# Kernel tuning notes

Hardware: AMD Instinct MI355X
Metric: run time of the kernel (lower is better)

## Reference

```python
import jax, jax.numpy as jnp
import numpy as np

# Grid derived from defaults: pc_range=(0,-40,-3,70.4,40,1), voxel=(0.2,0.2,4)
GX, GY = 352, 400          # round((70.4-0)/0.2), round((40-(-40))/0.2)
B, P = 4, 65536            # samples, points per sample
NSEG = B * GX * GY + 1     # dense pillar-id space + 1 sentinel for masked points
OUT_CH = 64
BN_EPS = 1e-3


def setup_inputs() -> dict:
    key = jax.random.key(0)
    k1, k2, k3 = jax.random.split(key, 3)
    xyz_min = jnp.array([0.0, -40.0, -3.0], jnp.float32)
    xyz_max = jnp.array([70.4, 40.0, 1.0], jnp.float32)
    xyz = jax.random.uniform(k1, (B, P, 3), jnp.float32, minval=xyz_min, maxval=xyz_max)
    rest = jax.random.normal(k2, (B, P, 4), jnp.float32)  # rcs, v_r, v_r_comp, time
    points = jnp.concatenate([xyz, rest], axis=-1)        # [B, P, 7]
    W = jax.random.normal(k3, (OUT_CH, 13), jnp.float32) * (1.0 / np.sqrt(13.0))
    gamma = jnp.ones((OUT_CH,), jnp.float32)
    beta = jnp.zeros((OUT_CH,), jnp.float32)
    return {"points": points, "W": W, "gamma": gamma, "beta": beta}


def reference(points, W, gamma, beta):
    Bn, Pn, _ = points.shape
    pts = points.reshape(Bn * Pn, 7)                      # [N, 7] (= torch points[:, 1:])
    dtype = pts.dtype
    voxel = jnp.array([0.2, 0.2, 4.0], dtype)
    pc_min = jnp.array([0.0, -40.0, -3.0], dtype)
    batch_idx = jnp.repeat(jnp.arange(Bn, dtype=jnp.int32), Pn)

    coords_f = (pts[:, :3] - pc_min) / voxel              # float voxel coords
    mask = ((coords_f[:, 0] >= 0) & (coords_f[:, 0] < GX)
            & (coords_f[:, 1] >= 0) & (coords_f[:, 1] < GY))
    coords = coords_f.astype(jnp.int32)                   # [N, 3] (cx, cy, cz)
    sentinel = Bn * GX * GY                               # trash segment for masked points
    lin = jnp.where(mask,
                    batch_idx * (GX * GY) + coords[:, 0] * GY + coords[:, 1],
                    sentinel)
    # torch.unique(..., return_inverse=True, dim=0) on (batch, cx, cy) rows ==
    # unique of the bijective linear id (same sorted order).
    unq, unq_inv = jnp.unique(lin, return_inverse=True, size=NSEG, fill_value=sentinel)

    cnt = jax.ops.segment_sum(jnp.ones((lin.shape[0], 1), dtype), unq_inv, num_segments=NSEG)
    mean_xyz = jax.ops.segment_sum(pts[:, :3], unq_inv, num_segments=NSEG) / jnp.maximum(cnt, 1.0)
    f_cluster = pts[:, :3] - mean_xyz[unq_inv]
    f_center = pts[:, :3] - (coords.astype(dtype) * voxel + voxel * 0.5 + pc_min)
    feats = jnp.concatenate([pts, f_cluster, f_center], axis=-1)   # [N, 13]

    # PFN layer (last_layer=True): Linear -> BN1d (training stats) -> ReLU
    x = feats @ W.T                                       # [N, 64]
    mu = x.mean(axis=0)
    var = x.var(axis=0)                                   # biased, as BN training
    x = jax.nn.relu((x - mu) * jax.lax.rsqrt(var + BN_EPS) * gamma + beta)

    fmax = jax.ops.segment_max(x, unq_inv, num_segments=NSEG)     # scatter_max
    x_max = fmax[unq_inv]                                 # gather back (PFN output)
    feat_max = jax.ops.segment_max(x_max, unq_inv, num_segments=NSEG)

    valid = (unq < sentinel)[:, None]                     # real pillars only
    feat_max = jnp.where(valid, feat_max, 0.0)            # padded/empty -> 0

    b = unq // (GX * GY)
    rem = unq % (GX * GY)
    cx = rem // GY
    cy = rem % GY
    coords_out = jnp.stack([b, cy, cx], axis=1).astype(jnp.int32)  # (batch, y, x)
    grid_size = jnp.array([GY, GX], jnp.int32)
    return feat_max, coords_out, grid_size
```

## Files before the change

### kernel.cpp

```cpp
#include <hip/hip_runtime.h>
#include <stdint.h>
#include <utility>

#define NPTS   262144
#define GXGY   140800
#define GYv    400
#define NSEG   563201
#define SENT   563200
#define NB_SCAN 275
#define PIL_BLOCKS 2048
#define MOM_BLOCKS 512

constexpr size_t alignup(size_t x) { return (x + 255) & ~(size_t)255; }
constexpr size_t O_CNT  = 0;
constexpr size_t O_SUMS = alignup(O_CNT + (size_t)NSEG * 4);
constexpr size_t O_MOM  = alignup(O_SUMS + (size_t)NSEG * 12);
constexpr size_t ZERO_BYTES = alignup(O_MOM + 104 * 4);
constexpr size_t O_PPTR = ZERO_BYTES;
constexpr size_t O_LINA = alignup(O_PPTR + (size_t)NSEG * 4);
constexpr size_t O_ROWI = alignup(O_LINA + (size_t)NPTS * 4);
constexpr size_t O_FEAT = alignup(O_ROWI + (size_t)NPTS * 16);
constexpr size_t O_BSO  = alignup(O_FEAT + (size_t)NPTS * 64);
constexpr size_t O_BSC  = alignup(O_BSO + NB_SCAN * 4);
constexpr size_t O_KP   = alignup(O_BSC + NB_SCAN * 4);
constexpr size_t O_WF   = alignup(O_KP + 256);
constexpr size_t O_SH   = alignup(O_WF + 832 * 4);

__device__ __forceinline__ int point_lin(float x, float y, int b, bool& mask) {
  float cxf = x / 0.2f;
  float cyf = (y + 40.0f) / 0.2f;
  int cx = (int)cxf, cy = (int)cyf;
  mask = (cxf >= 0.0f) && (cxf < 352.0f) && (cyf >= 0.0f) && (cyf < 400.0f);
  return mask ? (b * GXGY + cx * GYv + cy) : SENT;
}

__global__ __launch_bounds__(256) void k_count(const float* __restrict__ pts,
                                               unsigned int* __restrict__ cnt,
                                               float* __restrict__ sums,
                                               unsigned int* __restrict__ lina) {
  int i = blockIdx.x * 256 + threadIdx.x;
  if (i >= NPTS) return;
  const float* p = pts + (size_t)i * 7;
  float x = p[0], y = p[1], z = p[2];
  bool m;
  int lin = point_lin(x, y, i >> 16, m);
  lina[i] = (unsigned)lin;
  atomicAdd(&cnt[lin], 1u);
  atomicAdd(&sums[lin * 3 + 0], x);
  atomicAdd(&sums[lin * 3 + 1], y);
  atomicAdd(&sums[lin * 3 + 2], z);
}

__global__ __launch_bounds__(256) void k_scan1(const unsigned int* __restrict__ cnt,
                                               unsigned int* __restrict__ bso,
                                               unsigned int* __restrict__ bsc) {
  int t = threadIdx.x;
  int base = blockIdx.x * 2048 + t * 8;
  const uint4* c4 = (const uint4*)(cnt + base);
  uint4 a = c4[0], b = c4[1];
  unsigned so = (a.x > 0) + (a.y > 0) + (a.z > 0) + (a.w > 0) +
                (b.x > 0) + (b.y > 0) + (b.z > 0) + (b.w > 0);
  unsigned sc = a.x + a.y + a.z + a.w + b.x + b.y + b.z + b.w;
  for (int m = 1; m < 64; m <<= 1) { so += __shfl_xor(so, m); sc += __shfl_xor(sc, m); }
  __shared__ unsigned wo[4], wc[4];
  if ((t & 63) == 0) { wo[t >> 6] = so; wc[t >> 6] = sc; }
  __syncthreads();
  if (t == 0) {
    bso[blockIdx.x] = wo[0] + wo[1] + wo[2] + wo[3];
    bsc[blockIdx.x] = wc[0] + wc[1] + wc[2] + wc[3];
  }
}

__global__ __launch_bounds__(256) void k_scan3(const unsigned int* __restrict__ cnt,
                                               const unsigned int* __restrict__ bso,
                                               const unsigned int* __restrict__ bsc,
                                               uint4* __restrict__ rowinfo,
                                               unsigned int* __restrict__ pptr,
                                               unsigned int* __restrict__ kp) {
  int t = threadIdx.x;
  unsigned vo_m = 0, vc_m = 0, vo_a = 0;
  for (int e = t; e < NB_SCAN; e += 256) {
    unsigned o = bso[e], c = bsc[e];
    vo_a += o;
    if (e < (int)blockIdx.x) { vo_m += o; vc_m += c; }
  }
  for (int m = 1; m < 64; m <<= 1) {
    vo_m += __shfl_xor(vo_m, m);
    vc_m += __shfl_xor(vc_m, m);
    vo_a += __shfl_xor(vo_a, m);
  }
  __shared__ unsigned s0[4], s1[4], s2[4];
  int wv = t >> 6;
  if ((t & 63) == 0) { s0[wv] = vo_m; s1[wv] = vc_m; s2[wv] = vo_a; }
  __syncthreads();
  unsigned boo = s0[0] + s0[1] + s0[2] + s0[3];
  unsigned boc = s1[0] + s1[1] + s1[2] + s1[3];
  unsigned tot = s2[0] + s2[1] + s2[2] + s2[3];
  if (blockIdx.x == 0 && t == 0) *kp = tot;

  int base = blockIdx.x * 2048 + t * 8;
  const uint4* q = (const uint4*)(cnt + base);
  uint4 a = q[0], b = q[1];
  unsigned c[8] = {a.x, a.y, a.z, a.w, b.x, b.y, b.z, b.w};
  unsigned po[8], pc[8];
  unsigned so = 0, sc = 0;
#pragma unroll
  for (int k = 0; k < 8; k++) {
    po[k] = so; pc[k] = sc;
    so += (c[k] > 0); sc += c[k];
  }
  __shared__ unsigned sdo[256], sdc[256];
  __syncthreads();
  sdo[t] = so; sdc[t] = sc;
  __syncthreads();
  for (int off = 1; off < 256; off <<= 1) {
    unsigned ao = (t >= off) ? sdo[t - off] : 0u;
    unsigned ac = (t >= off) ? sdc[t - off] : 0u;
    __syncthreads();
    sdo[t] += ao; sdc[t] += ac;
    __syncthreads();
  }
  unsigned eo = sdo[t] - so + boo;
  unsigned ec = sdc[t] - sc + boc;
#pragma unroll
  for (int k = 0; k < 8; k++) {
    if (c[k] > 0) {
      unsigned r = eo + po[k];
      unsigned start = ec + pc[k];
      rowinfo[r] = make_uint4((unsigned)(base + k), start, c[k], 0u);
      pptr[base + k] = start;
    }
  }
}

__global__ __launch_bounds__(256) void k_sortfeat(const float* __restrict__ pts,
                                                  const unsigned int* __restrict__ lina,
                                                  const unsigned int* __restrict__ cnt,
                                                  const float* __restrict__ sums,
                                                  unsigned int* __restrict__ pptr,
                                                  float* __restrict__ feat) {
  int i = blockIdx.x * 256 + threadIdx.x;
  if (i >= NPTS) return;
  unsigned lin = lina[i];
  if (lin == SENT) return;
  const float* p = pts + (size_t)i * 7;
  float x = p[0], y = p[1], z = p[2];
  unsigned pos = atomicAdd(&pptr[lin], 1u);
  float cm = fmaxf((float)cnt[lin], 1.0f);
  float m0 = sums[lin * 3 + 0] / cm;
  float m1 = sums[lin * 3 + 1] / cm;
  float m2 = sums[lin * 3 + 2] / cm;
  int cx = (int)(x / 0.2f);
  int cy = (int)((y + 40.0f) / 0.2f);
  int cz = (int)((z + 3.0f) / 4.0f);
  float4 A = make_float4(x, y, z, p[3]);
  float4 B = make_float4(p[4], p[5], p[6], x - m0);
  float4 C = make_float4(y - m1, z - m2,
                         x - ((float)cx * 0.2f + 0.1f + 0.0f),
                         y - ((float)cy * 0.2f + 0.1f - 40.0f));
  float4 D = make_float4(z - ((float)cz * 4.0f + 2.0f - 3.0f), 0.f, 0.f, 0.f);
  float4* fb = (float4*)(feat + (size_t)pos * 16);
  fb[0] = A; fb[1] = B; fb[2] = C; fb[3] = D;
}

constexpr int tri_j(int t) { int j = 0; while (t >= 13 - j) { t -= 13 - j; j++; } return j; }
constexpr int tri_k(int t) { int j = 0; while (t >= 13 - j) { t -= 13 - j; j++; } return j + t; }

template<int G, size_t U>
__device__ __forceinline__ void accum_one(const float (&f)[13], float (&acc)[52]) {
  constexpr int E = G * 52 + (int)U;
  if constexpr (E < 13) {
    acc[U] += f[E];
  } else {
    constexpr int J = tri_j(E - 13);
    constexpr int K = tri_k(E - 13);
    acc[U] += f[J] * f[K];
  }
}
template<int G, size_t... Us>
__device__ __forceinline__ void accum_all(const float (&f)[13], float (&acc)[52],
                                          std::index_sequence<Us...>) {
  (accum_one<G, Us>(f, acc), ...);
}

template<int G>
__device__ __forceinline__ void moments_body(const float* __restrict__ feat,
                                             float* __restrict__ mom, int chunk) {
  float acc[52];
#pragma unroll
  for (int u = 0; u < 52; u++) acc[u] = 0.f;
#pragma unroll
  for (int r = 0; r < 4; r++) {
    int i = chunk * 1024 + r * 256 + threadIdx.x;
    const float4* fp = (const float4*)(feat + (size_t)i * 16);
    float4 A = fp[0], B = fp[1], C = fp[2], D = fp[3];
    float f[13] = {A.x, A.y, A.z, A.w, B.x, B.y, B.z, B.w, C.x, C.y, C.z, C.w, D.x};
    accum_all<G>(f, acc, std::make_index_sequence<52>{});
  }
  __shared__ float red[4][52];
  int wv = threadIdx.x >> 6, lane = threadIdx.x & 63;
#pragma unroll
  for (int u = 0; u < 52; u++) {
    float v = acc[u];
    v += __shfl_xor(v, 1);  v += __shfl_xor(v, 2);  v += __shfl_xor(v, 4);
    v += __shfl_xor(v, 8);  v += __shfl_xor(v, 16); v += __shfl_xor(v, 32);
    if (lane == 0) red[wv][u] = v;
  }
  __syncthreads();
  if (threadIdx.x < 52) {
    int u = threadIdx.x;
    atomicAdd(&mom[G * 52 + u], red[0][u] + red[1][u] + red[2][u] + red[3][u]);
  }
}

__global__ __launch_bounds__(256, 2) void k_moments(const float* __restrict__ feat,
                                                    float* __restrict__ mom) {
  int chunk = blockIdx.x >> 1;
  if ((blockIdx.x & 1) == 0) moments_body<0>(feat, mom, chunk);
  else                       moments_body<1>(feat, mom, chunk);
}

__global__ void k_bnfinal(const float* __restrict__ W,
                          const float* __restrict__ g,
                          const float* __restrict__ bta,
                          const float* __restrict__ mom,
                          float* __restrict__ wf,
                          float* __restrict__ sh) {
  int c = threadIdx.x;
  float w[13];
#pragma unroll
  for (int j = 0; j < 13; j++) w[j] = W[c * 13 + j];
  const float invN = 1.0f / (float)NPTS;
  float mu = 0.f;
#pragma unroll
  for (int j = 0; j < 13; j++) mu += w[j] * (mom[j] * invN);
  float e2 = 0.f;
  int mi = 13;
#pragma unroll
  for (int j = 0; j < 13; j++) {
#pragma unroll
    for (int k = j; k < 13; k++) {
      float coef = (j == k) ? 1.0f : 2.0f;
      e2 += coef * w[j] * w[k] * mom[mi];
      mi++;
    }
  }
  e2 *= invN;
  float var = e2 - mu * mu;
  float rsig = 1.0f / sqrtf(var + 1e-3f);
  float sc = g[c] * rsig;
#pragma unroll
  for (int j = 0; j < 13; j++) wf[c * 13 + j] = w[j] * sc;
  sh[c] = bta[c] - mu * sc;
}

__global__ __launch_bounds__(256) void k_pillar(const float* __restrict__ wf,
                                                const float* __restrict__ sh,
                                                const uint4* __restrict__ rowinfo,
                                                const unsigned int* __restrict__ kp_p,
                                                const float* __restrict__ feat,
                                                float* __restrict__ out) {
  int tid = threadIdx.x;
  int lane = tid & 15;
  int ch0 = lane * 4;
  float wr[52];
  float shv[4];
#pragma unroll
  for (int c4 = 0; c4 < 4; c4++) {
    shv[c4] = sh[ch0 + c4];
#pragma unroll
    for (int j = 0; j < 13; j++) wr[c4 * 13 + j] = wf[(ch0 + c4) * 13 + j];
  }
  unsigned kp = *kp_p;

  const int NGRP = PIL_BLOCKS * 16;
  for (int r = blockIdx.x * 16 + (tid >> 4); r < NSEG; r += NGRP) {
    float m0 = -3.4e38f, m1 = -3.4e38f, m2 = -3.4e38f, m3 = -3.4e38f;
    int b = 4, cy = 0, cx = 0;
    if ((unsigned)r < kp) {
      uint4 ri = rowinfo[r];
      unsigned id = ri.x, start = ri.y, n = ri.z;
      b = id / GXGY;
      unsigned rem = id - (unsigned)b * GXGY;
      cx = rem / GYv;
      cy = rem - cx * GYv;
      const float4* fb = (const float4*)(feat + (size_t)start * 16);
      for (unsigned p = 0; p < n; p++) {
        float4 A = fb[0], B = fb[1], C = fb[2], D = fb[3];
        fb += 4;
        float d0, d1, d2, d3;
#define DOT(dst, c4)                                                          \
        dst = shv[c4];                                                        \
        dst += wr[c4 * 13 + 0]  * A.x;  dst += wr[c4 * 13 + 1]  * A.y;        \
        dst += wr[c4 * 13 + 2]  * A.z;  dst += wr[c4 * 13 + 3]  * A.w;        \
        dst += wr[c4 * 13 + 4]  * B.x;  dst += wr[c4 * 13 + 5]  * B.y;        \
        dst += wr[c4 * 13 + 6]  * B.z;  dst += wr[c4 * 13 + 7]  * B.w;        \
        dst += wr[c4 * 13 + 8]  * C.x;  dst += wr[c4 * 13 + 9]  * C.y;        \
        dst += wr[c4 * 13 + 10] * C.z;  dst += wr[c4 * 13 + 11] * C.w;        \
        dst += wr[c4 * 13 + 12] * D.x;
        DOT(d0, 0) DOT(d1, 1) DOT(d2, 2) DOT(d3, 3)
#undef DOT
        m0 = fmaxf(m0, d0); m1 = fmaxf(m1, d1);
        m2 = fmaxf(m2, d2); m3 = fmaxf(m3, d3);
      }
    }
    float4 v = make_float4(fmaxf(m0, 0.f), fmaxf(m1, 0.f),
                           fmaxf(m2, 0.f), fmaxf(m3, 0.f));
    *(float4*)(out + (size_t)r * 64 + lane * 4) = v;
    if (lane == 0) {
      float* cc = out + (size_t)NSEG * 64 + (size_t)r * 3;
      cc[0] = (float)b;
      cc[1] = (float)cy;
      cc[2] = (float)cx;
    }
  }
  if (blockIdx.x == 0 && tid == 0) {
    float* g = out + (size_t)NSEG * 67;
    g[0] = 400.0f;
    g[1] = 352.0f;
  }
}

extern "C" void kernel_launch(void* const* d_in, const int* in_sizes, int n_in,
                              void* d_out, int out_size, void* d_ws, size_t ws_size,
                              hipStream_t stream) {
  const float* pts = (const float*)d_in[0];
  const float* W   = (const float*)d_in[1];
  const float* g   = (const float*)d_in[2];
  const float* bta = (const float*)d_in[3];
  float* out = (float*)d_out;
  char* ws = (char*)d_ws;

  unsigned int* cnt  = (unsigned int*)(ws + O_CNT);
  float*        sums = (float*)(ws + O_SUMS);
  float*        mom  = (float*)(ws + O_MOM);
  unsigned int* pptr = (unsigned int*)(ws + O_PPTR);
  unsigned int* lina = (unsigned int*)(ws + O_LINA);
  uint4*        rowi = (uint4*)(ws + O_ROWI);
  float*        feat = (float*)(ws + O_FEAT);
  unsigned int* bso  = (unsigned int*)(ws + O_BSO);
  unsigned int* bsc  = (unsigned int*)(ws + O_BSC);
  unsigned int* kp   = (unsigned int*)(ws + O_KP);
  float*        wf   = (float*)(ws + O_WF);
  float*        sh   = (float*)(ws + O_SH);
  (void)in_sizes; (void)n_in; (void)out_size; (void)ws_size;

  hipMemsetAsync(ws, 0, ZERO_BYTES, stream);

  k_count   <<<NPTS / 256, 256, 0, stream>>>(pts, cnt, sums, lina);
  k_scan1   <<<NB_SCAN, 256, 0, stream>>>(cnt, bso, bsc);
  k_scan3   <<<NB_SCAN, 256, 0, stream>>>(cnt, bso, bsc, rowi, pptr, kp);
  k_sortfeat<<<NPTS / 256, 256, 0, stream>>>(pts, lina, cnt, sums, pptr, feat);
  k_moments <<<MOM_BLOCKS, 256, 0, stream>>>(feat, mom);
  k_bnfinal <<<1, 64, 0, stream>>>(W, g, bta, mom, wf, sh);
  k_pillar  <<<PIL_BLOCKS, 256, 0, stream>>>(wf, sh, rowi, kp, feat, out);
}
```

Baseline: 286.9 us.

## Compute pillar means from sorted points and fold derived features into weights

Drops the float atomic scatter of xyz sums and the lina buffer. k_sortfeat now stores only the raw 7-channel point in a 32-byte record. Pillar means are computed per pillar inside the moments kernel, which walks sorted rows and rebuilds the 13 features on the fly. k_pillar folds the cluster and center offsets into per-pillar bias terms and combined weights, so each point needs fewer FMAs and half the feature bytes. The risk is load imbalance, because the moments kernel now iterates per pillar with a variable point count, and the float summation order changes.

```diff
diff --git a/kernel.cpp b/kernel.cpp
--- a/kernel.cpp
+++ b/kernel.cpp
@@ -9,18 +9,17 @@
 #define SENT   563200
 #define NB_SCAN 275
 #define PIL_BLOCKS 2048
-#define MOM_BLOCKS 512
+#define MOMG_BLOCKS 512
 
 constexpr size_t alignup(size_t x) { return (x + 255) & ~(size_t)255; }
 constexpr size_t O_CNT  = 0;
-constexpr size_t O_SUMS = alignup(O_CNT + (size_t)NSEG * 4);
-constexpr size_t O_MOM  = alignup(O_SUMS + (size_t)NSEG * 12);
+constexpr size_t O_MOM  = alignup(O_CNT + (size_t)NSEG * 4);
 constexpr size_t ZERO_BYTES = alignup(O_MOM + 104 * 4);
 constexpr size_t O_PPTR = ZERO_BYTES;
-constexpr size_t O_LINA = alignup(O_PPTR + (size_t)NSEG * 4);
-constexpr size_t O_ROWI = alignup(O_LINA + (size_t)NPTS * 4);
+constexpr size_t O_ROWI = alignup(O_PPTR + (size_t)NSEG * 4);
 constexpr size_t O_FEAT = alignup(O_ROWI + (size_t)NPTS * 16);
-constexpr size_t O_BSO  = alignup(O_FEAT + (size_t)NPTS * 64);
+constexpr size_t O_MEAN = alignup(O_FEAT + (size_t)NPTS * 32);
+constexpr size_t O_BSO  = alignup(O_MEAN + (size_t)NPTS * 12);
 constexpr size_t O_BSC  = alignup(O_BSO + NB_SCAN * 4);
 constexpr size_t O_KP   = alignup(O_BSC + NB_SCAN * 4);
 constexpr size_t O_WF   = alignup(O_KP + 256);
@@ -35,20 +34,14 @@
 }
 
 __global__ __launch_bounds__(256) void k_count(const float* __restrict__ pts,
-                                               unsigned int* __restrict__ cnt,
-                                               float* __restrict__ sums,
-                                               unsigned int* __restrict__ lina) {
+                                               unsigned int* __restrict__ cnt) {
   int i = blockIdx.x * 256 + threadIdx.x;
   if (i >= NPTS) return;
   const float* p = pts + (size_t)i * 7;
-  float x = p[0], y = p[1], z = p[2];
+  float x = p[0], y = p[1];
   bool m;
   int lin = point_lin(x, y, i >> 16, m);
-  lina[i] = (unsigned)lin;
   atomicAdd(&cnt[lin], 1u);
-  atomicAdd(&sums[lin * 3 + 0], x);
-  atomicAdd(&sums[lin * 3 + 1], y);
-  atomicAdd(&sums[lin * 3 + 2], z);
 }
 
 __global__ __launch_bounds__(256) void k_scan1(const unsigned int* __restrict__ cnt,
@@ -134,33 +127,19 @@
 }
 
 __global__ __launch_bounds__(256) void k_sortfeat(const float* __restrict__ pts,
-                                                  const unsigned int* __restrict__ lina,
-                                                  const unsigned int* __restrict__ cnt,
-                                                  const float* __restrict__ sums,
                                                   unsigned int* __restrict__ pptr,
                                                   float* __restrict__ feat) {
   int i = blockIdx.x * 256 + threadIdx.x;
   if (i >= NPTS) return;
-  unsigned lin = lina[i];
-  if (lin == SENT) return;
   const float* p = pts + (size_t)i * 7;
   float x = p[0], y = p[1], z = p[2];
+  bool m;
+  int lin = point_lin(x, y, i >> 16, m);
+  if (lin == SENT) return;
   unsigned pos = atomicAdd(&pptr[lin], 1u);
-  float cm = fmaxf((float)cnt[lin], 1.0f);
-  float m0 = sums[lin * 3 + 0] / cm;
-  float m1 = sums[lin * 3 + 1] / cm;
-  float m2 = sums[lin * 3 + 2] / cm;
-  int cx = (int)(x / 0.2f);
-  int cy = (int)((y + 40.0f) / 0.2f);
-  int cz = (int)((z + 3.0f) / 4.0f);
-  float4 A = make_float4(x, y, z, p[3]);
-  float4 B = make_float4(p[4], p[5], p[6], x - m0);
-  float4 C = make_float4(y - m1, z - m2,
-                         x - ((float)cx * 0.2f + 0.1f + 0.0f),
-                         y - ((float)cy * 0.2f + 0.1f - 40.0f));
-  float4 D = make_float4(z - ((float)cz * 4.0f + 2.0f - 3.0f), 0.f, 0.f, 0.f);
-  float4* fb = (float4*)(feat + (size_t)pos * 16);
-  fb[0] = A; fb[1] = B; fb[2] = C; fb[3] = D;
+  float4* fb = (float4*)(feat + (size_t)pos * 8);
+  fb[0] = make_float4(x, y, z, p[3]);
+  fb[1] = make_float4(p[4], p[5], p[6], 0.0f);
 }
 
 constexpr int tri_j(int t) { int j = 0; while (t >= 13 - j) { t -= 13 - j; j++; } return j; }
@@ -184,18 +163,41 @@
 }
 
 template<int G>
-__device__ __forceinline__ void moments_body(const float* __restrict__ feat,
-                                             float* __restrict__ mom, int chunk) {
+__device__ __forceinline__ void momrank_body(const uint4* __restrict__ rowinfo,
+                                             const float* __restrict__ feat,
+                                             float* __restrict__ meanr,
+                                             float* __restrict__ mom,
+                                             unsigned kp) {
   float acc[52];
 #pragma unroll
   for (int u = 0; u < 52; u++) acc[u] = 0.f;
-#pragma unroll
-  for (int r = 0; r < 4; r++) {
-    int i = chunk * 1024 + r * 256 + threadIdx.x;
-    const float4* fp = (const float4*)(feat + (size_t)i * 16);
-    float4 A = fp[0], B = fp[1], C = fp[2], D = fp[3];
-    float f[13] = {A.x, A.y, A.z, A.w, B.x, B.y, B.z, B.w, C.x, C.y, C.z, C.w, D.x};
-    accum_all<G>(f, acc, std::make_index_sequence<52>{});
+  const unsigned stride = MOMG_BLOCKS * 256;
+  for (unsigned r = (blockIdx.x >> 1) * 256 + threadIdx.x; r < kp; r += stride) {
+    uint4 ri = rowinfo[r];
+    unsigned start = ri.y, n = ri.z;
+    const float4* fp = (const float4*)(feat + (size_t)start * 8);
+    float sx = 0.f, sy = 0.f, sz = 0.f;
+    for (unsigned p = 0; p < n; p++) { float4 A = fp[2 * p]; sx += A.x; sy += A.y; sz += A.z; }
+    float inv = 1.0f / fmaxf((float)n, 1.0f);
+    float mx = sx * inv, my = sy * inv, mz = sz * inv;
+    if (G == 0) {
+      meanr[(size_t)r * 3 + 0] = mx;
+      meanr[(size_t)r * 3 + 1] = my;
+      meanr[(size_t)r * 3 + 2] = mz;
+    }
+    for (unsigned p = 0; p < n; p++) {
+      float4 A = fp[2 * p], Bq = fp[2 * p + 1];
+      float x = A.x, y = A.y, z = A.z;
+      int cx = (int)(x / 0.2f);
+      int cy = (int)((y + 40.0f) / 0.2f);
+      int cz = (int)((z + 3.0f) / 4.0f);
+      float f[13] = {x, y, z, A.w, Bq.x, Bq.y, Bq.z,
+                     x - mx, y - my, z - mz,
+                     x - ((float)cx * 0.2f + 0.1f + 0.0f),
+                     y - ((float)cy * 0.2f + 0.1f - 40.0f),
+                     z - ((float)cz * 4.0f + 2.0f - 3.0f)};
+      accum_all<G>(f, acc, std::make_index_sequence<52>{});
+    }
   }
   __shared__ float red[4][52];
   int wv = threadIdx.x >> 6, lane = threadIdx.x & 63;
@@ -213,11 +215,14 @@
   }
 }
 
-__global__ __launch_bounds__(256, 2) void k_moments(const float* __restrict__ feat,
-                                                    float* __restrict__ mom) {
-  int chunk = blockIdx.x >> 1;
-  if ((blockIdx.x & 1) == 0) moments_body<0>(feat, mom, chunk);
-  else                       moments_body<1>(feat, mom, chunk);
+__global__ __launch_bounds__(256, 2) void k_momrank(const uint4* __restrict__ rowinfo,
+                                                    const float* __restrict__ feat,
+                                                    float* __restrict__ meanr,
+                                                    float* __restrict__ mom,
+                                                    const unsigned int* __restrict__ kpp) {
+  unsigned kp = *kpp;
+  if ((blockIdx.x & 1) == 0) momrank_body<0>(rowinfo, feat, meanr, mom, kp);
+  else                       momrank_body<1>(rowinfo, feat, meanr, mom, kp);
 }
 
 __global__ void k_bnfinal(const float* __restrict__ W,
@@ -259,17 +264,21 @@
                                                 const uint4* __restrict__ rowinfo,
                                                 const unsigned int* __restrict__ kp_p,
                                                 const float* __restrict__ feat,
+                                                const float* __restrict__ meanr,
                                                 float* __restrict__ out) {
   int tid = threadIdx.x;
   int lane = tid & 15;
   int ch0 = lane * 4;
   float wr[52];
-  float shv[4];
+  float shv[4], wx[4], wy[4], wz[4];
 #pragma unroll
   for (int c4 = 0; c4 < 4; c4++) {
     shv[c4] = sh[ch0 + c4];
 #pragma unroll
     for (int j = 0; j < 13; j++) wr[c4 * 13 + j] = wf[(ch0 + c4) * 13 + j];
+    wx[c4] = wr[c4 * 13 + 0] + wr[c4 * 13 + 7] + wr[c4 * 13 + 10];
+    wy[c4] = wr[c4 * 13 + 1] + wr[c4 * 13 + 8] + wr[c4 * 13 + 11];
+    wz[c4] = wr[c4 * 13 + 2] + wr[c4 * 13 + 9];
   }
   unsigned kp = *kp_p;
 
@@ -284,20 +293,31 @@
       unsigned rem = id - (unsigned)b * GXGY;
       cx = rem / GYv;
       cy = rem - cx * GYv;
-      const float4* fb = (const float4*)(feat + (size_t)start * 16);
+      float gx = (float)cx * 0.2f + 0.1f;
+      float gy = (float)cy * 0.2f + 0.1f - 40.0f;
+      float mx = meanr[(size_t)r * 3 + 0];
+      float my = meanr[(size_t)r * 3 + 1];
+      float mz = meanr[(size_t)r * 3 + 2];
+      float s0_[4];
+#pragma unroll
+      for (int c4 = 0; c4 < 4; c4++) {
+        s0_[c4] = shv[c4] - wr[c4 * 13 + 7] * mx - wr[c4 * 13 + 8] * my
+                          - wr[c4 * 13 + 9] * mz - wr[c4 * 13 + 10] * gx
+                          - wr[c4 * 13 + 11] * gy;
+      }
+      const float4* fb = (const float4*)(feat + (size_t)start * 8);
       for (unsigned p = 0; p < n; p++) {
-        float4 A = fb[0], B = fb[1], C = fb[2], D = fb[3];
-        fb += 4;
+        float4 A = fb[0], Bq = fb[1];
+        fb += 2;
+        int cz = (int)((A.z + 3.0f) / 4.0f);
+        float fz = A.z - ((float)cz * 4.0f + 2.0f - 3.0f);
         float d0, d1, d2, d3;
 #define DOT(dst, c4)                                                          \
-        dst = shv[c4];                                                        \
-        dst += wr[c4 * 13 + 0]  * A.x;  dst += wr[c4 * 13 + 1]  * A.y;        \
-        dst += wr[c4 * 13 + 2]  * A.z;  dst += wr[c4 * 13 + 3]  * A.w;        \
-        dst += wr[c4 * 13 + 4]  * B.x;  dst += wr[c4 * 13 + 5]  * B.y;        \
-        dst += wr[c4 * 13 + 6]  * B.z;  dst += wr[c4 * 13 + 7]  * B.w;        \
-        dst += wr[c4 * 13 + 8]  * C.x;  dst += wr[c4 * 13 + 9]  * C.y;        \
-        dst += wr[c4 * 13 + 10] * C.z;  dst += wr[c4 * 13 + 11] * C.w;        \
-        dst += wr[c4 * 13 + 12] * D.x;
+        dst = s0_[c4];                                                        \
+        dst += wx[c4] * A.x;            dst += wy[c4] * A.y;                  \
+        dst += wz[c4] * A.z;            dst += wr[c4 * 13 + 3] * A.w;         \
+        dst += wr[c4 * 13 + 4] * Bq.x;  dst += wr[c4 * 13 + 5] * Bq.y;        \
+        dst += wr[c4 * 13 + 6] * Bq.z;  dst += wr[c4 * 13 + 12] * fz;
         DOT(d0, 0) DOT(d1, 1) DOT(d2, 2) DOT(d3, 3)
 #undef DOT
         m0 = fmaxf(m0, d0); m1 = fmaxf(m1, d1);
@@ -315,9 +335,9 @@
     }
   }
   if (blockIdx.x == 0 && tid == 0) {
-    float* g = out + (size_t)NSEG * 67;
-    g[0] = 400.0f;
-    g[1] = 352.0f;
+    float* g2 = out + (size_t)NSEG * 67;
+    g2[0] = 400.0f;
+    g2[1] = 352.0f;
   }
 }
 
@@ -332,12 +352,11 @@
   char* ws = (char*)d_ws;
 
   unsigned int* cnt  = (unsigned int*)(ws + O_CNT);
-  float*        sums = (float*)(ws + O_SUMS);
   float*        mom  = (float*)(ws + O_MOM);
   unsigned int* pptr = (unsigned int*)(ws + O_PPTR);
-  unsigned int* lina = (unsigned int*)(ws + O_LINA);
   uint4*        rowi = (uint4*)(ws + O_ROWI);
   float*        feat = (float*)(ws + O_FEAT);
+  float*        mnr  = (float*)(ws + O_MEAN);
   unsigned int* bso  = (unsigned int*)(ws + O_BSO);
   unsigned int* bsc  = (unsigned int*)(ws + O_BSC);
   unsigned int* kp   = (unsigned int*)(ws + O_KP);
@@ -347,11 +366,11 @@
 
   hipMemsetAsync(ws, 0, ZERO_BYTES, stream);
 
-  k_count   <<<NPTS / 256, 256, 0, stream>>>(pts, cnt, sums, lina);
+  k_count   <<<NPTS / 256, 256, 0, stream>>>(pts, cnt);
   k_scan1   <<<NB_SCAN, 256, 0, stream>>>(cnt, bso, bsc);
   k_scan3   <<<NB_SCAN, 256, 0, stream>>>(cnt, bso, bsc, rowi, pptr, kp);
-  k_sortfeat<<<NPTS / 256, 256, 0, stream>>>(pts, lina, cnt, sums, pptr, feat);
-  k_moments <<<MOM_BLOCKS, 256, 0, stream>>>(feat, mom);
+  k_sortfeat<<<NPTS / 256, 256, 0, stream>>>(pts, pptr, feat);
+  k_momrank <<<2 * MOMG_BLOCKS, 256, 0, stream>>>(rowi, feat, mnr, mom, kp);
   k_bnfinal <<<1, 64, 0, stream>>>(W, g, bta, mom, wf, sh);
-  k_pillar  <<<PIL_BLOCKS, 256, 0, stream>>>(wf, sh, rowi, kp, feat, out);
-}
+  k_pillar  <<<PIL_BLOCKS, 256, 0, stream>>>(wf, sh, rowi, kp, feat, mnr, out);
+}
```

Measured after the change: 256.0 us. -10.7%, faster.
